# Optimization experiments

Hardware: AMD Instinct MI355X
Metric: run time of the kernel (lower is better)

The kernel has to match this reference:

```python
import jax, jax.numpy as jnp
import numpy as np

NUM_RBF = 16
MAX_REL = 32
TOP_K = 48
RBF_D_MIN, RBF_D_MAX = 2.0, 22.0
CB_A, CB_B, CB_C = -0.58273431, 0.56802827, -0.54067466
LN_EPS = 1e-5


def gather_L(x, idx):
    # x: (B, L, ...)  idx: (B, L, K) -> (B, L, K, ...): neighbors along L per batch
    return jax.vmap(lambda xb, ib: xb[ib])(x, idx)


def rbf_encode(D):
    mu = jnp.linspace(RBF_D_MIN, RBF_D_MAX, NUM_RBF, dtype=D.dtype)  # (16,)
    sigma = (RBF_D_MAX - RBF_D_MIN) / NUM_RBF
    return jnp.exp(-((D[..., None] - mu) / sigma) ** 2)


def setup_inputs() -> dict:
    key = jax.random.key(0)
    ks = jax.random.split(key, 4)
    B, L = 4, 2048
    num_pos, hidden = 16, 128
    X = jax.random.normal(ks[0], (B, L, 4, 3), jnp.float32) * 3.0
    residue_mask = jnp.ones((B, L), jnp.float32)
    R_idx = jnp.tile(jnp.arange(L, dtype=jnp.int32)[None, :], (B, 1))
    chain_labels = jnp.zeros((B, L), jnp.int32)
    W_pos = jax.random.normal(ks[1], (2 * MAX_REL + 2, num_pos), jnp.float32) * 0.1
    b_pos = jnp.zeros((num_pos,), jnp.float32)
    W_edge = jax.random.normal(ks[2], (25 * NUM_RBF + num_pos, hidden), jnp.float32) * 0.05
    ln_gamma = jnp.ones((hidden,), jnp.float32)
    ln_beta = jnp.zeros((hidden,), jnp.float32)
    return dict(X=X, residue_mask=residue_mask, R_idx=R_idx, chain_labels=chain_labels,
                W_pos=W_pos, b_pos=b_pos, W_edge=W_edge, ln_gamma=ln_gamma, ln_beta=ln_beta)


def reference(X, residue_mask, R_idx, chain_labels, W_pos, b_pos, W_edge, ln_gamma, ln_beta):
    B, L = X.shape[:2]
    # virtual CB from N, CA, C
    N, CA, C = X[..., 0, :], X[..., 1, :], X[..., 2, :]
    b = CA - N
    c = C - CA
    a = jnp.cross(b, c)
    CB = CB_A * a + CB_B * b + CB_C * c + CA                      # (B, L, 3)
    atoms_5 = jnp.concatenate([X, CB[:, :, None, :]], axis=-2)    # (B, L, 5, 3)

    # kNN on CA-CA squared distances, masked columns pushed far away
    diff = CA[:, :, None, :] - CA[:, None, :, :]                  # (B, L, L, 3)
    dist_sq = jnp.sum(diff ** 2, axis=-1)
    dist_sq = dist_sq + (1.0 - residue_mask)[:, None, :] * 1e6
    _, E_idx = jax.lax.top_k(-dist_sq, TOP_K)                     # smallest-k -> (B, L, K)

    # 25 atom-pair RBF features
    X_g = gather_L(atoms_5, E_idx)                                # (B, L, K, 5, 3)
    D = jnp.sqrt(jnp.sum((atoms_5[:, :, None, :, None, :]
                          - X_g[:, :, :, None, :, :]) ** 2, axis=-1) + 1e-6)  # (B,L,K,5,5)
    rbf = rbf_encode(D).reshape(B, L, TOP_K, 25 * NUM_RBF)        # (B, L, K, 400)

    # positional encodings (ProteinMPNN style)
    R_g = gather_L(R_idx, E_idx)                                  # (B, L, K)
    C_g = gather_L(chain_labels, E_idx)
    offset = R_idx[:, :, None] - R_g
    same_chain = (chain_labels[:, :, None] == C_g).astype(jnp.int32)
    d = jnp.clip(offset + MAX_REL, 0, 2 * MAX_REL) * same_chain + (1 - same_chain) * (2 * MAX_REL + 1)
    d_onehot = jax.nn.one_hot(d, 2 * MAX_REL + 2, dtype=W_pos.dtype)  # (B, L, K, 66)
    pos_enc = jnp.einsum('blkc,cp->blkp', d_onehot, W_pos) + b_pos    # (B, L, K, 16)

    edge_input = jnp.concatenate([pos_enc, rbf], axis=-1)         # (B, L, K, 416)
    E = jnp.einsum('blkc,ch->blkh', edge_input, W_edge)           # (B, L, K, 128)
    mean = jnp.mean(E, axis=-1, keepdims=True)
    var = jnp.var(E, axis=-1, keepdims=True)
    E = (E - mean) * jax.lax.rsqrt(var + LN_EPS) * ln_gamma + ln_beta
    return E_idx, E
```

## Files before the change

### kernel.cpp

```cpp
#include <hip/hip_runtime.h>
#include <hip/hip_bf16.h>

#define BB 4
#define LL 2048
#define KK 48
#define HH 128
#define CANDCAP 384
#define FSTR 40
#define DLT 1.06666666667f
#define BINSCALE 2.0f

using bf16x8 = __attribute__((ext_vector_type(8))) short;
using f32x4  = __attribute__((ext_vector_type(4))) float;
using u64x2  = __attribute__((ext_vector_type(2))) unsigned long long;

__global__ __launch_bounds__(256) void pf15_prep_w(
    const float* __restrict__ Wedge, const float* __restrict__ Wpos,
    const float* __restrict__ bpos, short* __restrict__ Wt) {
    int idx = blockIdx.x * 256 + threadIdx.x;
    if (idx >= 16 * 8 * 16 * 32) return;
    int j  = idx & 7;
    int kg = (idx >> 3) & 3;
    int col = (idx >> 5) & 15;
    int nt = (idx >> 9) & 7;
    int kt = idx >> 12;
    int k = kt * 32 + kg * 8 + j;
    int n = nt * 16 + col;
    float v = 0.0f;
    if (kt < 13) {
        if (k < 400) v = Wedge[(size_t)(16 + k) * HH + n];
    } else {
        int d = k - 416;
        if (d < 66) {
            float s = 0.f;
            #pragma unroll
            for (int p = 0; p < 16; ++p)
                s += (Wpos[d * 16 + p] + bpos[p]) * Wedge[p * HH + n];
            v = s;
        }
    }
    __hip_bfloat16 h = __float2bfloat16(v);
    Wt[idx] = *reinterpret_cast<short*>(&h);
}

__global__ __launch_bounds__(256) void pf15_prep_ca(const float* __restrict__ X,
                                                    const float* __restrict__ mask,
                                                    float4* __restrict__ caq) {
    int i = blockIdx.x * 256 + threadIdx.x;
    if (i >= BB * LL) return;
    const float* x = X + (size_t)i * 12;
    float bias = __fmul_rn(1.0f - mask[i], 1.0e6f);
    caq[i] = make_float4(x[3], x[4], x[5], bias);
}

__global__ __launch_bounds__(256, 6) void pf15_main(
    const float* __restrict__ X,
    const int* __restrict__ Ridx, const int* __restrict__ chain,
    const float* __restrict__ gamma, const float* __restrict__ beta,
    const short* __restrict__ Wt, const float4* __restrict__ caq,
    float* __restrict__ outIdx, float* __restrict__ outEdge) {

    const int row = blockIdx.x;
    const int bq = row >> 11, lq = row & (LL - 1);
    const int tid = threadIdx.x;
    const int lane = tid & 63, wid = tid >> 6;
    const float* Xb = X + (size_t)bq * LL * 12;
    const float4* caqb = caq + (size_t)bq * LL;

    __shared__ __align__(16) union {
        int hist[1024];
        unsigned long long cand[CANDCAP];
        float geo[KK * 15 + 16];
    } uA;
    __shared__ float sD[KK * 25];
    __shared__ __align__(16) short sFeat[2][KK * FSTR];
    __shared__ float sGB[2 * HH];
    __shared__ float sPartS[KK][4], sPartSS[KK][4];
    __shared__ float sMean[KK], sInv[KK];
    __shared__ int sSel[KK], sDcode[KK];
    __shared__ int sWsum[4];
    __shared__ int sBstar, sCc;

    if (tid < HH) { sGB[tid * 2] = gamma[tid]; sGB[tid * 2 + 1] = beta[tid]; }

    const float4 sc = caqb[lq];
    float dval[8];
    #pragma unroll
    for (int i = 0; i < 8; ++i) {
        float4 q = caqb[i * 256 + tid];
        float dx = __fadd_rn(sc.x, -q.x);
        float dy = __fadd_rn(sc.y, -q.y);
        float dz = __fadd_rn(sc.z, -q.z);
        float d2 = __fadd_rn(__fadd_rn(__fmul_rn(dx, dx), __fmul_rn(dy, dy)),
                             __fmul_rn(dz, dz));
        dval[i] = __fadd_rn(d2, q.w);
    }

    *reinterpret_cast<int4*>(&uA.hist[tid * 4]) = make_int4(0, 0, 0, 0);
    if (tid == 0) sCc = 0;
    __syncthreads();
    #pragma unroll
    for (int i = 0; i < 8; ++i) {
        int bin = (int)(dval[i] * BINSCALE);
        bin = bin > 1023 ? 1023 : bin;
        atomicAdd(&uA.hist[bin], 1);
    }
    __syncthreads();

    int c0 = uA.hist[tid * 4 + 0];
    int c1 = uA.hist[tid * 4 + 1];
    int c2 = uA.hist[tid * 4 + 2];
    int c3 = uA.hist[tid * 4 + 3];
    int local = c0 + c1 + c2 + c3;
    int v = local;
    #pragma unroll
    for (int off = 1; off < 64; off <<= 1) {
        int o = __shfl_up(v, off, 64);
        if (lane >= off) v += o;
    }
    if (lane == 63) sWsum[wid] = v;
    __syncthreads();
    int woff = 0;
    #pragma unroll
    for (int w2 = 0; w2 < 4; ++w2) if (w2 < wid) woff += sWsum[w2];
    int incl = woff + v, excl = incl - local;
    if (excl < KK && incl >= KK) {
        int cum = excl, b = tid * 4;
        if (cum + c0 >= KK) sBstar = b;
        else { cum += c0;
            if (cum + c1 >= KK) sBstar = b + 1;
            else { cum += c1;
                if (cum + c2 >= KK) sBstar = b + 2;
                else sBstar = b + 3; } }
    }
    __syncthreads();

    int bstar = sBstar;
    #pragma unroll
    for (int i = 0; i < 8; ++i) {
        int bin = (int)(dval[i] * BINSCALE);
        bin = bin > 1023 ? 1023 : bin;
        if (bin <= bstar) {
            int pos = atomicAdd(&sCc, 1);
            if (pos < CANDCAP)
                uA.cand[pos] =
                    ((unsigned long long)__float_as_uint(dval[i]) << 32)
                    | (unsigned)(i * 256 + tid);
        }
    }
    __syncthreads();

    int C = sCc < CANDCAP ? sCc : CANDCAP;
    for (int ci = tid; ci < C; ci += 256) {
        unsigned long long me = uA.cand[ci];
        int rank = 0, j2 = 0;
        int Cv = C & ~7;
        for (; j2 < Cv; j2 += 8) {
            u64x2 q0 = *reinterpret_cast<u64x2*>(&uA.cand[j2]);
            u64x2 q1 = *reinterpret_cast<u64x2*>(&uA.cand[j2 + 2]);
            u64x2 q2 = *reinterpret_cast<u64x2*>(&uA.cand[j2 + 4]);
            u64x2 q3 = *reinterpret_cast<u64x2*>(&uA.cand[j2 + 6]);
            rank += (q0[0] < me) + (q0[1] < me) + (q1[0] < me) + (q1[1] < me)
                  + (q2[0] < me) + (q2[1] < me) + (q3[0] < me) + (q3[1] < me);
        }
        for (; j2 < C; ++j2) rank += (uA.cand[j2] < me) ? 1 : 0;
        if (rank < KK) sSel[rank] = (int)(me & 0xFFFFFFFFu);
    }
    __syncthreads();

    if (tid < KK) outIdx[(size_t)row * KK + tid] = (float)sSel[tid];

    const float KA = -0.58273431f, KB2 = 0.56802827f, KC = -0.54067466f;
    if (tid < KK) {
        int j = sSel[tid];
        const float* x = Xb + (size_t)j * 12;
        float u0 = x[3] - x[0], u1 = x[4] - x[1], u2 = x[5] - x[2];
        float w0 = x[6] - x[3], w1 = x[7] - x[4], w2 = x[8] - x[5];
        float r0 = u1 * w2 - u2 * w1;
        float r1 = u2 * w0 - u0 * w2;
        float r2 = u0 * w1 - u1 * w0;
        float* o = &uA.geo[tid * 15];
        #pragma unroll
        for (int t = 0; t < 12; ++t) o[t] = x[t];
        o[12] = KA * r0 + KB2 * u0 + KC * w0 + x[3];
        o[13] = KA * r1 + KB2 * u1 + KC * w1 + x[4];
        o[14] = KA * r2 + KB2 * u2 + KC * w2 + x[5];
        int offr = Ridx[row] - Ridx[(size_t)bq * LL + j];
        int same = (chain[row] == chain[(size_t)bq * LL + j]);
        int d = offr + 32;
        d = d < 0 ? 0 : (d > 64 ? 64 : d);
        sDcode[tid] = same ? d : 65;
    }
    if (tid == 64) {
        const float* x = Xb + (size_t)lq * 12;
        float u0 = x[3] - x[0], u1 = x[4] - x[1], u2 = x[5] - x[2];
        float w0 = x[6] - x[3], w1 = x[7] - x[4], w2 = x[8] - x[5];
        float r0 = u1 * w2 - u2 * w1;
        float r1 = u2 * w0 - u0 * w2;
        float r2 = u0 * w1 - u1 * w0;
        float* s = &uA.geo[720];
        #pragma unroll
        for (int t = 0; t < 12; ++t) s[t] = x[t];
        s[12] = KA * r0 + KB2 * u0 + KC * w0 + x[3];
        s[13] = KA * r1 + KB2 * u1 + KC * w1 + x[4];
        s[14] = KA * r2 + KB2 * u2 + KC * w2 + x[5];
    }
    __syncthreads();

    #pragma unroll
    for (int it = 0; it < 6; ++it) {
        int idx = it * 256 + tid;
        int k = idx >> 5, pq = idx & 31;
        if (pq < 25) {
            int p = pq / 5, q = pq % 5;
            float dx = uA.geo[720 + p * 3 + 0] - uA.geo[k * 15 + q * 3 + 0];
            float dy = uA.geo[720 + p * 3 + 1] - uA.geo[k * 15 + q * 3 + 1];
            float dz = uA.geo[720 + p * 3 + 2] - uA.geo[k * 15 + q * 3 + 2];
            sD[k * 25 + pq] = sqrtf(dx * dx + dy * dy + dz * dz + 1e-6f);
        }
    }
    __syncthreads();

    auto feat_compute = [&](int kt, int fb) {
        if (tid < 192) {
            int pair = tid >> 1, half = tid & 1;
            int k = pair >> 1, pq_lo = pair & 1;
            int pq = kt * 2 + pq_lo;
            bf16x8 ov;
            if (pq < 25) {
                float Dv = sD[k * 25 + pq];
                float t0 = (Dv - 2.0f) * 0.8f;
                float tm = __builtin_fmaf(-(float)(half << 3), DLT, t0);
                #pragma unroll
                for (int mi = 0; mi < 8; ++mi) {
                    float val = __expf(-tm * tm);
                    __hip_bfloat16 hb = __float2bfloat16(val);
                    ov[mi] = *reinterpret_cast<short*>(&hb);
                    tm -= DLT;
                }
            } else {
                #pragma unroll
                for (int mi = 0; mi < 8; ++mi) ov[mi] = 0;
            }
            *reinterpret_cast<bf16x8*>(
                &sFeat[fb][k * FSTR + pq_lo * 16 + (half << 3)]) = ov;
        }
    };

    feat_compute(0, 0);
    __syncthreads();

    f32x4 acc[3][2];
    #pragma unroll
    for (int mt = 0; mt < 3; ++mt)
        #pragma unroll
        for (int nb = 0; nb < 2; ++nb) acc[mt][nb] = (f32x4){0.f, 0.f, 0.f, 0.f};
    const int nt0 = wid * 2;
    const int arow = lane & 15, kg = lane >> 4;

    int cur = 0;
    #pragma unroll 1
    for (int kt = 0; kt < 13; ++kt) {
        const short* wp = Wt + (((size_t)(kt * 8 + nt0) * 16 + arow) * 32 + kg * 8);
        bf16x8 b0 = *reinterpret_cast<const bf16x8*>(wp);
        bf16x8 b1 = *reinterpret_cast<const bf16x8*>(wp + 16 * 32);
        if (kt + 1 < 13) feat_compute(kt + 1, cur ^ 1);
        bf16x8 a0 = *reinterpret_cast<const bf16x8*>(&sFeat[cur][(arow     ) * FSTR + kg * 8]);
        bf16x8 a1 = *reinterpret_cast<const bf16x8*>(&sFeat[cur][(arow + 16) * FSTR + kg * 8]);
        bf16x8 a2 = *reinterpret_cast<const bf16x8*>(&sFeat[cur][(arow + 32) * FSTR + kg * 8]);
        acc[0][0] = __builtin_amdgcn_mfma_f32_16x16x32_bf16(a0, b0, acc[0][0], 0, 0, 0);
        acc[1][0] = __builtin_amdgcn_mfma_f32_16x16x32_bf16(a1, b0, acc[1][0], 0, 0, 0);
        acc[2][0] = __builtin_amdgcn_mfma_f32_16x16x32_bf16(a2, b0, acc[2][0], 0, 0, 0);
        acc[0][1] = __builtin_amdgcn_mfma_f32_16x16x32_bf16(a0, b1, acc[0][1], 0, 0, 0);
        acc[1][1] = __builtin_amdgcn_mfma_f32_16x16x32_bf16(a1, b1, acc[1][1], 0, 0, 0);
        acc[2][1] = __builtin_amdgcn_mfma_f32_16x16x32_bf16(a2, b1, acc[2][1], 0, 0, 0);
        if (kt + 1 < 13) { __syncthreads(); cur ^= 1; }
    }

    int dc0 = sDcode[arow], dc1 = sDcode[arow + 16], dc2 = sDcode[arow + 32];
    #pragma unroll 1
    for (int kp = 0; kp < 3; ++kp) {
        int base = kp * 32 + kg * 8;
        bf16x8 a0, a1, a2;
        #pragma unroll
        for (int j = 0; j < 8; ++j) {
            a0[j] = (dc0 == base + j) ? (short)0x3F80 : (short)0;
            a1[j] = (dc1 == base + j) ? (short)0x3F80 : (short)0;
            a2[j] = (dc2 == base + j) ? (short)0x3F80 : (short)0;
        }
        const short* wp = Wt + (((size_t)((13 + kp) * 8 + nt0) * 16 + arow) * 32 + kg * 8);
        bf16x8 b0 = *reinterpret_cast<const bf16x8*>(wp);
        bf16x8 b1 = *reinterpret_cast<const bf16x8*>(wp + 16 * 32);
        acc[0][0] = __builtin_amdgcn_mfma_f32_16x16x32_bf16(a0, b0, acc[0][0], 0, 0, 0);
        acc[1][0] = __builtin_amdgcn_mfma_f32_16x16x32_bf16(a1, b0, acc[1][0], 0, 0, 0);
        acc[2][0] = __builtin_amdgcn_mfma_f32_16x16x32_bf16(a2, b0, acc[2][0], 0, 0, 0);
        acc[0][1] = __builtin_amdgcn_mfma_f32_16x16x32_bf16(a0, b1, acc[0][1], 0, 0, 0);
        acc[1][1] = __builtin_amdgcn_mfma_f32_16x16x32_bf16(a1, b1, acc[1][1], 0, 0, 0);
        acc[2][1] = __builtin_amdgcn_mfma_f32_16x16x32_bf16(a2, b1, acc[2][1], 0, 0, 0);
    }

    #pragma unroll
    for (int mt = 0; mt < 3; ++mt)
        #pragma unroll
        for (int r = 0; r < 4; ++r) {
            float s = acc[mt][0][r] + acc[mt][1][r];
            float ss = acc[mt][0][r] * acc[mt][0][r]
                     + acc[mt][1][r] * acc[mt][1][r];
            s  += __shfl_xor(s, 1, 64);  ss += __shfl_xor(ss, 1, 64);
            s  += __shfl_xor(s, 2, 64);  ss += __shfl_xor(ss, 2, 64);
            s  += __shfl_xor(s, 4, 64);  ss += __shfl_xor(ss, 4, 64);
            s  += __shfl_xor(s, 8, 64);  ss += __shfl_xor(ss, 8, 64);
            if (arow == 0) {
                int e = mt * 16 + kg * 4 + r;
                sPartS[e][wid] = s;
                sPartSS[e][wid] = ss;
            }
        }
    __syncthreads();
    if (tid < KK) {
        float s = sPartS[tid][0] + sPartS[tid][1] + sPartS[tid][2] + sPartS[tid][3];
        float ss = sPartSS[tid][0] + sPartSS[tid][1] + sPartSS[tid][2] + sPartSS[tid][3];
        float mean = s * (1.0f / 128.0f);
        float var = ss * (1.0f / 128.0f) - mean * mean;
        sMean[tid] = mean;
        sInv[tid] = 1.0f / sqrtf(var + 1e-5f);
    }
    __syncthreads();

    const int col0 = nt0 * 16 + arow, col1 = col0 + 16;
    const float g0 = sGB[col0 * 2], be0 = sGB[col0 * 2 + 1];
    const float g1 = sGB[col1 * 2], be1 = sGB[col1 * 2 + 1];
    float* outR = outEdge + (size_t)row * KK * HH;
    #pragma unroll
    for (int mt = 0; mt < 3; ++mt)
        #pragma unroll
        for (int r = 0; r < 4; ++r) {
            int e = mt * 16 + kg * 4 + r;
            float mean = sMean[e], inv = sInv[e];
            outR[(size_t)e * HH + col0] = (acc[mt][0][r] - mean) * inv * g0 + be0;
            outR[(size_t)e * HH + col1] = (acc[mt][1][r] - mean) * inv * g1 + be1;
        }
}

extern "C" void kernel_launch(void* const* d_in, const int* in_sizes, int n_in,
                              void* d_out, int out_size, void* d_ws, size_t ws_size,
                              hipStream_t stream) {
    const float* X     = (const float*)d_in[0];
    const float* mask  = (const float*)d_in[1];
    const int*   Ridx  = (const int*)d_in[2];
    const int*   chain = (const int*)d_in[3];
    const float* Wpos  = (const float*)d_in[4];
    const float* bpos  = (const float*)d_in[5];
    const float* Wedge = (const float*)d_in[6];
    const float* gamma = (const float*)d_in[7];
    const float* beta  = (const float*)d_in[8];

    float* outBase = (float*)d_out;
    float* outIdx  = outBase;
    float* outEdge = outBase + (size_t)BB * LL * KK;

    short*  Wt  = (short*)d_ws;
    float4* caq = (float4*)((char*)d_ws + 16 * 8 * 16 * 32 * 2);

    hipLaunchKernelGGL(pf15_prep_w, dim3(256), dim3(256), 0, stream,
                       Wedge, Wpos, bpos, Wt);
    hipLaunchKernelGGL(pf15_prep_ca, dim3((BB * LL + 255) / 256), dim3(256), 0,
                       stream, X, mask, caq);
    hipLaunchKernelGGL(pf15_main, dim3(BB * LL), dim3(256), 0, stream,
                       X, Ridx, chain, gamma, beta, Wt, caq, outIdx, outEdge);
}
```

Measured before the change: 134.9 us.

## Double K-step per RBF pipeline stage and use incremental exp2 recurrence

The RBF-feature/MFMA pipeline now handles 64 K columns (four atom pairs) per stage instead of 32. This halves the number of block-wide barriers, from 12 to 6 plus a tail step, and spreads feature generation over all 256 threads instead of 192. Gaussian evaluation switches from __expf(-t^2) per bin to exp2f on an exponent updated by first and second differences, which cuts the per-bin multiplies. The feature buffer stride grows to 72, raising LDS use, and the running-difference exponent may accumulate small rounding error before the bf16 cast.

```diff
diff --git a/kernel.cpp b/kernel.cpp
--- a/kernel.cpp
+++ b/kernel.cpp
@@ -6,15 +6,20 @@
 #define KK 48
 #define HH 128
 #define CANDCAP 384
-#define FSTR 40
+#define FSTR 72
 #define DLT 1.06666666667f
 #define BINSCALE 2.0f
+#define L2E 1.44269504089f
+#define D1A 3.07774901f
+#define D1B 1.64147055f
+#define D2C -3.28294110f
 
 using bf16x8 = __attribute__((ext_vector_type(8))) short;
+using bf16x4 = __attribute__((ext_vector_type(4))) short;
 using f32x4  = __attribute__((ext_vector_type(4))) float;
 using u64x2  = __attribute__((ext_vector_type(2))) unsigned long long;
 
-__global__ __launch_bounds__(256) void pf15_prep_w(
+__global__ __launch_bounds__(256) void pf16_prep_w(
     const float* __restrict__ Wedge, const float* __restrict__ Wpos,
     const float* __restrict__ bpos, short* __restrict__ Wt) {
     int idx = blockIdx.x * 256 + threadIdx.x;
@@ -43,7 +48,7 @@
     Wt[idx] = *reinterpret_cast<short*>(&h);
 }
 
-__global__ __launch_bounds__(256) void pf15_prep_ca(const float* __restrict__ X,
+__global__ __launch_bounds__(256) void pf16_prep_ca(const float* __restrict__ X,
                                                     const float* __restrict__ mask,
                                                     float4* __restrict__ caq) {
     int i = blockIdx.x * 256 + threadIdx.x;
@@ -53,7 +58,7 @@
     caq[i] = make_float4(x[3], x[4], x[5], bias);
 }
 
-__global__ __launch_bounds__(256, 6) void pf15_main(
+__global__ __launch_bounds__(256, 6) void pf16_main(
     const float* __restrict__ X,
     const int* __restrict__ Ridx, const int* __restrict__ chain,
     const float* __restrict__ gamma, const float* __restrict__ beta,
@@ -222,28 +227,33 @@
     __syncthreads();
 
     auto feat_compute = [&](int kt, int fb) {
-        if (tid < 192) {
-            int pair = tid >> 1, half = tid & 1;
-            int k = pair >> 1, pq_lo = pair & 1;
-            int pq = kt * 2 + pq_lo;
-            bf16x8 ov;
+        #pragma unroll
+        for (int i = 0; i < 3; ++i) {
+            int q = tid + i * 256;
+            int k = q >> 4;
+            int rem = q & 15;
+            int pql = rem >> 2, mq = rem & 3;
+            int pq = kt * 4 + pql;
+            bf16x4 ov;
             if (pq < 25) {
                 float Dv = sD[k * 25 + pq];
-                float t0 = (Dv - 2.0f) * 0.8f;
-                float tm = __builtin_fmaf(-(float)(half << 3), DLT, t0);
+                float tm = __builtin_fmaf(-(float)(mq << 2), DLT,
+                                          (Dv - 2.0f) * 0.8f);
+                float g  = -(tm * tm) * L2E;
+                float d1 = __builtin_fmaf(D1A, tm, -D1B);
                 #pragma unroll
-                for (int mi = 0; mi < 8; ++mi) {
-                    float val = __expf(-tm * tm);
+                for (int mi = 0; mi < 4; ++mi) {
+                    float val = exp2f(g);
+                    g += d1; d1 += D2C;
                     __hip_bfloat16 hb = __float2bfloat16(val);
                     ov[mi] = *reinterpret_cast<short*>(&hb);
-                    tm -= DLT;
                 }
             } else {
                 #pragma unroll
-                for (int mi = 0; mi < 8; ++mi) ov[mi] = 0;
+                for (int mi = 0; mi < 4; ++mi) ov[mi] = 0;
             }
-            *reinterpret_cast<bf16x8*>(
-                &sFeat[fb][k * FSTR + pq_lo * 16 + (half << 3)]) = ov;
+            *reinterpret_cast<bf16x4*>(
+                &sFeat[fb][k * FSTR + pql * 16 + (mq << 2)]) = ov;
         }
     };
 
@@ -257,24 +267,55 @@
         for (int nb = 0; nb < 2; ++nb) acc[mt][nb] = (f32x4){0.f, 0.f, 0.f, 0.f};
     const int nt0 = wid * 2;
     const int arow = lane & 15, kg = lane >> 4;
+    const short* wpBase = Wt + (((size_t)nt0 * 16 + arow) * 32 + kg * 8);
+    const int K32S = 8 * 16 * 32;
 
     int cur = 0;
     #pragma unroll 1
-    for (int kt = 0; kt < 13; ++kt) {
-        const short* wp = Wt + (((size_t)(kt * 8 + nt0) * 16 + arow) * 32 + kg * 8);
-        bf16x8 b0 = *reinterpret_cast<const bf16x8*>(wp);
-        bf16x8 b1 = *reinterpret_cast<const bf16x8*>(wp + 16 * 32);
-        if (kt + 1 < 13) feat_compute(kt + 1, cur ^ 1);
-        bf16x8 a0 = *reinterpret_cast<const bf16x8*>(&sFeat[cur][(arow     ) * FSTR + kg * 8]);
-        bf16x8 a1 = *reinterpret_cast<const bf16x8*>(&sFeat[cur][(arow + 16) * FSTR + kg * 8]);
-        bf16x8 a2 = *reinterpret_cast<const bf16x8*>(&sFeat[cur][(arow + 32) * FSTR + kg * 8]);
+    for (int kt = 0; kt < 6; ++kt) {
+        const short* wpA = wpBase + (size_t)(2 * kt) * K32S;
+        bf16x8 b00 = *reinterpret_cast<const bf16x8*>(wpA);
+        bf16x8 b10 = *reinterpret_cast<const bf16x8*>(wpA + 16 * 32);
+        bf16x8 b01 = *reinterpret_cast<const bf16x8*>(wpA + K32S);
+        bf16x8 b11 = *reinterpret_cast<const bf16x8*>(wpA + K32S + 16 * 32);
+        feat_compute(kt + 1, cur ^ 1);
+        const short* fb = &sFeat[cur][0];
+        bf16x8 a00 = *reinterpret_cast<const bf16x8*>(&fb[(arow     ) * FSTR + kg * 8]);
+        bf16x8 a10 = *reinterpret_cast<const bf16x8*>(&fb[(arow + 16) * FSTR + kg * 8]);
+        bf16x8 a20 = *reinterpret_cast<const bf16x8*>(&fb[(arow + 32) * FSTR + kg * 8]);
+        bf16x8 a01 = *reinterpret_cast<const bf16x8*>(&fb[(arow     ) * FSTR + 32 + kg * 8]);
+        bf16x8 a11 = *reinterpret_cast<const bf16x8*>(&fb[(arow + 16) * FSTR + 32 + kg * 8]);
+        bf16x8 a21 = *reinterpret_cast<const bf16x8*>(&fb[(arow + 32) * FSTR + 32 + kg * 8]);
+        acc[0][0] = __builtin_amdgcn_mfma_f32_16x16x32_bf16(a00, b00, acc[0][0], 0, 0, 0);
+        acc[1][0] = __builtin_amdgcn_mfma_f32_16x16x32_bf16(a10, b00, acc[1][0], 0, 0, 0);
+        acc[2][0] = __builtin_amdgcn_mfma_f32_16x16x32_bf16(a20, b00, acc[2][0], 0, 0, 0);
+        acc[0][1] = __builtin_amdgcn_mfma_f32_16x16x32_bf16(a00, b10, acc[0][1], 0, 0, 0);
+        acc[1][1] = __builtin_amdgcn_mfma_f32_16x16x32_bf16(a10, b10, acc[1][1], 0, 0, 0);
+        acc[2][1] = __builtin_amdgcn_mfma_f32_16x16x32_bf16(a20, b10, acc[2][1], 0, 0, 0);
+        acc[0][0] = __builtin_amdgcn_mfma_f32_16x16x32_bf16(a01, b01, acc[0][0], 0, 0, 0);
+        acc[1][0] = __builtin_amdgcn_mfma_f32_16x16x32_bf16(a11, b01, acc[1][0], 0, 0, 0);
+        acc[2][0] = __builtin_amdgcn_mfma_f32_16x16x32_bf16(a21, b01, acc[2][0], 0, 0, 0);
+        acc[0][1] = __builtin_amdgcn_mfma_f32_16x16x32_bf16(a01, b11, acc[0][1], 0, 0, 0);
+        acc[1][1] = __builtin_amdgcn_mfma_f32_16x16x32_bf16(a11, b11, acc[1][1], 0, 0, 0);
+        acc[2][1] = __builtin_amdgcn_mfma_f32_16x16x32_bf16(a21, b11, acc[2][1], 0, 0, 0);
+        __syncthreads();
+        cur ^= 1;
+    }
+
+    {
+        const short* wpA = wpBase + (size_t)12 * K32S;
+        bf16x8 b0 = *reinterpret_cast<const bf16x8*>(wpA);
+        bf16x8 b1 = *reinterpret_cast<const bf16x8*>(wpA + 16 * 32);
+        const short* fb = &sFeat[cur][0];
+        bf16x8 a0 = *reinterpret_cast<const bf16x8*>(&fb[(arow     ) * FSTR + kg * 8]);
+        bf16x8 a1 = *reinterpret_cast<const bf16x8*>(&fb[(arow + 16) * FSTR + kg * 8]);
+        bf16x8 a2 = *reinterpret_cast<const bf16x8*>(&fb[(arow + 32) * FSTR + kg * 8]);
         acc[0][0] = __builtin_amdgcn_mfma_f32_16x16x32_bf16(a0, b0, acc[0][0], 0, 0, 0);
         acc[1][0] = __builtin_amdgcn_mfma_f32_16x16x32_bf16(a1, b0, acc[1][0], 0, 0, 0);
         acc[2][0] = __builtin_amdgcn_mfma_f32_16x16x32_bf16(a2, b0, acc[2][0], 0, 0, 0);
         acc[0][1] = __builtin_amdgcn_mfma_f32_16x16x32_bf16(a0, b1, acc[0][1], 0, 0, 0);
         acc[1][1] = __builtin_amdgcn_mfma_f32_16x16x32_bf16(a1, b1, acc[1][1], 0, 0, 0);
         acc[2][1] = __builtin_amdgcn_mfma_f32_16x16x32_bf16(a2, b1, acc[2][1], 0, 0, 0);
-        if (kt + 1 < 13) { __syncthreads(); cur ^= 1; }
     }
 
     int dc0 = sDcode[arow], dc1 = sDcode[arow + 16], dc2 = sDcode[arow + 32];
@@ -288,7 +329,7 @@
             a1[j] = (dc1 == base + j) ? (short)0x3F80 : (short)0;
             a2[j] = (dc2 == base + j) ? (short)0x3F80 : (short)0;
         }
-        const short* wp = Wt + (((size_t)((13 + kp) * 8 + nt0) * 16 + arow) * 32 + kg * 8);
+        const short* wp = wpBase + (size_t)(13 + kp) * K32S;
         bf16x8 b0 = *reinterpret_cast<const bf16x8*>(wp);
         bf16x8 b1 = *reinterpret_cast<const bf16x8*>(wp + 16 * 32);
         acc[0][0] = __builtin_amdgcn_mfma_f32_16x16x32_bf16(a0, b0, acc[0][0], 0, 0, 0);
@@ -362,10 +403,10 @@
     short*  Wt  = (short*)d_ws;
     float4* caq = (float4*)((char*)d_ws + 16 * 8 * 16 * 32 * 2);
 
-    hipLaunchKernelGGL(pf15_prep_w, dim3(256), dim3(256), 0, stream,
+    hipLaunchKernelGGL(pf16_prep_w, dim3(256), dim3(256), 0, stream,
                        Wedge, Wpos, bpos, Wt);
-    hipLaunchKernelGGL(pf15_prep_ca, dim3((BB * LL + 255) / 256), dim3(256), 0,
+    hipLaunchKernelGGL(pf16_prep_ca, dim3((BB * LL + 255) / 256), dim3(256), 0,
                        stream, X, mask, caq);
-    hipLaunchKernelGGL(pf15_main, dim3(BB * LL), dim3(256), 0, stream,
+    hipLaunchKernelGGL(pf16_main, dim3(BB * LL), dim3(256), 0, stream,
                        X, Ridx, chain, gamma, beta, Wt, caq, outIdx, outEdge);
 }
```

Measured after the change: 140.5 us. 4.1% more time.
